# Kernel optimization log

Measured on AMD Instinct MI355X. Metric: run time of the kernel, lower is better.

Reference implementation:

```python
import jax, jax.numpy as jnp
import numpy as np

N_NODES = 100000


def setup_inputs() -> dict:
    key = jax.random.key(0)
    ks = jax.random.split(key, 6)
    x = jax.random.normal(ks[0], (N_NODES, 128), dtype=jnp.float32)
    edge_index = jax.random.randint(ks[1], (2, 1600000), 0, N_NODES, dtype=jnp.int32)
    W_gcn = jax.random.normal(ks[2], (128, 128), dtype=jnp.float32) * 0.05
    b_gcn = jax.random.normal(ks[3], (128,), dtype=jnp.float32) * 0.05
    W_fc = jax.random.normal(ks[4], (64, 128), dtype=jnp.float32) * 0.05
    b_fc = jax.random.normal(ks[5], (64,), dtype=jnp.float32) * 0.05
    return {"x": x, "edge_index": edge_index, "W_gcn": W_gcn, "b_gcn": b_gcn, "W_fc": W_fc, "b_fc": b_fc}


def _gcn_conv(x, edge_index, W, b):
    N = x.shape[0]
    # add self-loops (PyG GCNConv default add_self_loops=True)
    loops = jnp.arange(N, dtype=edge_index.dtype)
    row = jnp.concatenate([edge_index[0], loops])  # source
    col = jnp.concatenate([edge_index[1], loops])  # target (aggregation index)
    # symmetric normalization: deg computed at target with unit edge weights
    deg = jax.ops.segment_sum(jnp.ones_like(col, dtype=x.dtype), col, num_segments=N)
    deg_inv_sqrt = jnp.where(deg > 0, jax.lax.rsqrt(deg), 0.0)
    norm = deg_inv_sqrt[row] * deg_inv_sqrt[col]  # [E+N]
    xw = x @ W  # [N, nhid] - transform before aggregation
    msgs = norm[:, None] * xw[row]  # gather + scale, [E+N, nhid]
    out = jax.ops.segment_sum(msgs, col, num_segments=N)  # scatter-add
    return out + b


def reference(x, edge_index, W_gcn, b_gcn, W_fc, b_fc):
    h = _gcn_conv(x, edge_index, W_gcn, b_gcn)  # [N, nhid]
    return h @ W_fc.T + b_fc  # [N, nclass]
```

## Files before the change

kernel.cpp:

```cpp
#include <hip/hip_runtime.h>
#include <hip/hip_bf16.h>

typedef __hip_bfloat16 bf16;

#define N_NODES 100000
#define N_EDGES 1600000
#define F_IN    128
#define F_OUT   64
#define NBLK    391

#define NB_BKT   196
#define BKT_SH   9
#define BKT_CAP  8960
#define LBIN_CAP 56
#define EPB_A    4096


__device__ __forceinline__ float ldf(const void* p, size_t i, bool isbf) {
    return isbf ? __bfloat162float(((const bf16*)p)[i]) : ((const float*)p)[i];
}
__device__ __forceinline__ void stf(void* p, size_t i, bool isbf, float v) {
    if (isbf) ((bf16*)p)[i] = __float2bfloat16(v);
    else      ((float*)p)[i] = v;
}
__device__ __forceinline__ unsigned short f2bfu(float f) {
    __hip_bfloat16 h = __float2bfloat16(f);
    union { __hip_bfloat16 h; unsigned short u; } c; c.h = h; return c.u;
}
__device__ __forceinline__ float bflo(unsigned int u) { return __uint_as_float(u << 16); }
__device__ __forceinline__ float bfhi(unsigned int u) { return __uint_as_float(u & 0xffff0000u); }

__global__ void k_detect(const unsigned short* __restrict__ w, int* __restrict__ flag) {
    int l = threadIdx.x;
    int good = 0;
#pragma unroll
    for (int q = 0; q < 2; ++q) {
        unsigned short v = w[2 * (l + 64 * q)];
        int e = (v >> 7) & 0xFF;
        if ((e >= 100 && e <= 140) || ((v & 0x7FFF) == 0)) good++;
    }
    unsigned long long m1 = __ballot(good >= 1), m2 = __ballot(good >= 2);
    if (l == 0) *flag = (__popcll(m1) + __popcll(m2) >= 96) ? 1 : 0;
}

__global__ void k_weights(const int* __restrict__ flag,
                          const void* __restrict__ Wg, const void* __restrict__ bg,
                          const void* __restrict__ Wf, const void* __restrict__ bfc,
                          float* __restrict__ M, float* __restrict__ cvec) {
    bool isbf = (*flag != 0);
    int t = blockIdx.x * blockDim.x + threadIdx.x;
    if (t >= F_IN * F_OUT) return;
    int k = t >> 6, c = t & 63;
    float s = 0.f;
    for (int j = 0; j < F_IN; ++j)
        s += ldf(Wg, k * F_IN + j, isbf) * ldf(Wf, c * F_IN + j, isbf);
    M[k * F_OUT + c] = s;
    if (k == 0) {
        float cs = ldf(bfc, c, isbf);
        for (int j = 0; j < F_IN; ++j)
            cs += ldf(bg, j, isbf) * ldf(Wf, c * F_IN + j, isbf);
        cvec[c] = cs;
    }
}


__global__ void k_zero(int* __restrict__ gtail) {
    int i = threadIdx.x;
    if (i < NB_BKT) gtail[i] = 0;
}

__global__ __launch_bounds__(256) void k_binA(const int* __restrict__ ei,
                                              int* __restrict__ gtail,
                                              unsigned* __restrict__ bkt) {
    __shared__ unsigned lbin[NB_BKT * LBIN_CAP];
    __shared__ int lcnt[NB_BKT];
    __shared__ int lbase[NB_BKT];
    int t = threadIdx.x;
    for (int b = t; b < NB_BKT; b += 256) lcnt[b] = 0;
    __syncthreads();
    int e0 = blockIdx.x * EPB_A;
#pragma unroll
    for (int q = 0; q < EPB_A / 256; ++q) {
        int e = e0 + q * 256 + t;
        if (e < N_EDGES) {
            int r = ei[e], c = ei[N_EDGES + e];
            int b = c >> BKT_SH;
            unsigned val = (unsigned)r | ((unsigned)(c & ((1 << BKT_SH) - 1)) << 17);
            int p = atomicAdd(&lcnt[b], 1);
            if (p < LBIN_CAP) {
                lbin[b * LBIN_CAP + p] = val;
            } else {
                int gp = atomicAdd(&gtail[b], 1);
                if (gp < BKT_CAP) bkt[(size_t)b * BKT_CAP + gp] = val;
            }
        }
    }
    __syncthreads();
    for (int b = t; b < NB_BKT; b += 256) {
        int n = min(lcnt[b], LBIN_CAP);
        lbase[b] = atomicAdd(&gtail[b], n);
    }
    __syncthreads();
    int w = t >> 6, l = t & 63;
    for (int b = w; b < NB_BKT; b += 4) {
        int nB = min(lcnt[b], LBIN_CAP);
        int gp0 = lbase[b];
        for (int i = l; i < nB; i += 64) {
            int gp = gp0 + i;
            if (gp < BKT_CAP) bkt[(size_t)b * BKT_CAP + gp] = lbin[b * LBIN_CAP + i];
        }
    }
}

__global__ void k_bktscan(const int* __restrict__ gtail, int* __restrict__ bbase) {
    __shared__ int sm[256];
    int t = threadIdx.x;
    int v = (t < NB_BKT) ? min(gtail[t], BKT_CAP) : 0;
    sm[t] = v; __syncthreads();
    for (int s = 1; s < 256; s <<= 1) {
        int add = (t >= s) ? sm[t - s] : 0;
        __syncthreads();
        sm[t] += add;
        __syncthreads();
    }
    if (t < NB_BKT) bbase[t] = sm[t] - v;
}

__global__ __launch_bounds__(512) void k_build(const unsigned* __restrict__ bkt,
                                               const int* __restrict__ gtail,
                                               const int* __restrict__ bbase,
                                               int* __restrict__ ptr,
                                               int* __restrict__ cnt,
                                               float* __restrict__ dinv,
                                               int* __restrict__ srcs) {
    __shared__ int cntl[512], sm[512], fill[512];
    int b = blockIdx.x, t = threadIdx.x;
    int n = min(gtail[b], BKT_CAP);
    int base = bbase[b];
    cntl[t] = 0;
    __syncthreads();
    for (int i = t; i < n; i += 512)
        atomicAdd(&cntl[bkt[(size_t)b * BKT_CAP + i] >> 17], 1);
    __syncthreads();
    int v = cntl[t];
    sm[t] = v; __syncthreads();
    for (int s = 1; s < 512; s <<= 1) {
        int add = (t >= s) ? sm[t - s] : 0;
        __syncthreads();
        sm[t] += add;
        __syncthreads();
    }
    int excl = sm[t] - v;
    fill[t] = excl;
    int node = (b << BKT_SH) + t;
    if (node < N_NODES) {
        ptr[node]  = base + excl;
        cnt[node]  = v;
        dinv[node] = rsqrtf((float)(v + 1));
    }
    __syncthreads();
    for (int i = t; i < n; i += 512) {
        unsigned e = bkt[(size_t)b * BKT_CAP + i];
        int c = (int)(e >> 17);
        int p = atomicAdd(&fill[c], 1);
        srcs[base + p] = (int)(e & 0x1FFFF);
    }
}

__global__ __launch_bounds__(256) void k_xmz(const int* __restrict__ flag,
                                             const void* __restrict__ x,
                                             const float* __restrict__ M,
                                             const float* __restrict__ dinv,
                                             bf16* __restrict__ y) {
    __shared__ float4 Ms4[F_IN * 16];
    __shared__ float4 xs4[32 * 64];
    int t = threadIdx.x;
    bool isbf = (*flag != 0);
    int r0 = blockIdx.x * 64;

#pragma unroll
    for (int q = 0; q < 8; ++q) {
        int i = q * 256 + t;
        Ms4[i] = ((const float4*)M)[i];
    }
    if (isbf) {
        const unsigned short* xb = (const unsigned short*)x;
#pragma unroll
        for (int q = 0; q < 4; ++q) {
            int idx = q * 256 + t;
            int row = idx >> 4, c8 = idx & 15;
            int rr = min(r0 + row, N_NODES - 1);
            uint4 u = ((const uint4*)(xb + (size_t)rr * F_IN))[c8];
            float4 v0 = make_float4(bflo(u.x), bfhi(u.x), bflo(u.y), bfhi(u.y));
            float4 v1 = make_float4(bflo(u.z), bfhi(u.z), bflo(u.w), bfhi(u.w));
            int k40 = c8 * 2, k41 = c8 * 2 + 1;
            xs4[k40 * 64 + (row ^ (k40 & 7))] = v0;
            xs4[k41 * 64 + (row ^ (k41 & 7))] = v1;
        }
    } else {
        const float* xf = (const float*)x;
#pragma unroll
        for (int q = 0; q < 8; ++q) {
            int idx = q * 256 + t;
            int row = idx >> 5, k4 = idx & 31;
            int rr = min(r0 + row, N_NODES - 1);
            float4 v = ((const float4*)(xf + (size_t)rr * F_IN))[k4];
            xs4[k4 * 64 + (row ^ (k4 & 7))] = v;
        }
    }
    __syncthreads();

    int cg = t & 15;
    int rs = t >> 4;
    float4 a0 = {0,0,0,0}, a1 = {0,0,0,0}, a2 = {0,0,0,0}, a3 = {0,0,0,0};

    for (int k4 = 0; k4 < 32; ++k4) {
        float4 m0 = Ms4[(k4 * 4 + 0) * 16 + cg];
        float4 m1 = Ms4[(k4 * 4 + 1) * 16 + cg];
        float4 m2 = Ms4[(k4 * 4 + 2) * 16 + cg];
        float4 m3 = Ms4[(k4 * 4 + 3) * 16 + cg];
        int sw = k4 & 7;
#pragma unroll
        for (int i = 0; i < 4; ++i) {
            int row = rs * 4 + i;
            float4 xv = xs4[k4 * 64 + (row ^ sw)];
            float4* a = (i == 0) ? &a0 : (i == 1) ? &a1 : (i == 2) ? &a2 : &a3;
            a->x += xv.x * m0.x + xv.y * m1.x + xv.z * m2.x + xv.w * m3.x;
            a->y += xv.x * m0.y + xv.y * m1.y + xv.z * m2.y + xv.w * m3.y;
            a->z += xv.x * m0.z + xv.y * m1.z + xv.z * m2.z + xv.w * m3.z;
            a->w += xv.x * m0.w + xv.y * m1.w + xv.z * m2.w + xv.w * m3.w;
        }
    }

    float4 av[4] = {a0, a1, a2, a3};
#pragma unroll
    for (int i = 0; i < 4; ++i) {
        int row = r0 + rs * 4 + i;
        if (row < N_NODES) {
            float d = dinv[row];
            ushort4 pk;
            pk.x = f2bfu(av[i].x * d); pk.y = f2bfu(av[i].y * d);
            pk.z = f2bfu(av[i].z * d); pk.w = f2bfu(av[i].w * d);
            ((ushort4*)((unsigned short*)y + (size_t)row * F_OUT))[cg] = pk;
        }
    }
}

__global__ __launch_bounds__(256) void k_agg(const int* __restrict__ flag,
                                             const int* __restrict__ ptr,
                                             const int* __restrict__ cnt,
                                             const int* __restrict__ srcs,
                                             const float* __restrict__ dinv,
                                             const bf16* __restrict__ y,
                                             const float* __restrict__ cvec,
                                             void* __restrict__ out) {
    int wid  = (blockIdx.x * 256 + threadIdx.x) >> 6;
    int lane = threadIdx.x & 63;
    int g  = lane >> 3;
    int j8 = lane & 7;
    int node = wid * 8 + g;
    bool alive = node < N_NODES;
    int n = 0, start = 0;
    if (alive) { n = cnt[node]; start = ptr[node]; }
    const uint4* y4 = (const uint4*)y;

    float acc[8];
#pragma unroll
    for (int i = 0; i < 8; ++i) acc[i] = 0.f;

    for (int b = 0; __any(b < n); b += 8) {
        int s = 0;
        int idx = b + j8;
        if (idx < n) s = srcs[start + idx];
#pragma unroll
        for (int k = 0; k < 8; ++k) {
            int su = __shfl(s, (g << 3) | k, 64);
            if (b + k < n) {
                uint4 v = y4[(size_t)su * 8 + j8];
                acc[0] += bflo(v.x); acc[1] += bfhi(v.x);
                acc[2] += bflo(v.y); acc[3] += bfhi(v.y);
                acc[4] += bflo(v.z); acc[5] += bfhi(v.z);
                acc[6] += bflo(v.w); acc[7] += bfhi(v.w);
            }
        }
    }

    if (!alive) return;
    bool isbf = (*flag != 0);
    uint4 sv = y4[(size_t)node * 8 + j8];
    float dn = dinv[node];
    const float4* cv4 = (const float4*)cvec;
    float4 c0 = cv4[j8 * 2], c1 = cv4[j8 * 2 + 1];
    size_t ob = (size_t)node * F_OUT + j8 * 8;
    if (isbf) {
        ushort4 p0, p1;
        p0.x = f2bfu(dn * (acc[0] + bflo(sv.x)) + c0.x);
        p0.y = f2bfu(dn * (acc[1] + bfhi(sv.x)) + c0.y);
        p0.z = f2bfu(dn * (acc[2] + bflo(sv.y)) + c0.z);
        p0.w = f2bfu(dn * (acc[3] + bfhi(sv.y)) + c0.w);
        p1.x = f2bfu(dn * (acc[4] + bflo(sv.z)) + c1.x);
        p1.y = f2bfu(dn * (acc[5] + bfhi(sv.z)) + c1.y);
        p1.z = f2bfu(dn * (acc[6] + bflo(sv.w)) + c1.z);
        p1.w = f2bfu(dn * (acc[7] + bfhi(sv.w)) + c1.w);
        ushort4* ob4 = (ushort4*)((unsigned short*)out + ob);
        ob4[0] = p0; ob4[1] = p1;
    } else {
        float4 q0, q1;
        q0.x = dn * (acc[0] + bflo(sv.x)) + c0.x;
        q0.y = dn * (acc[1] + bfhi(sv.x)) + c0.y;
        q0.z = dn * (acc[2] + bflo(sv.y)) + c0.z;
        q0.w = dn * (acc[3] + bfhi(sv.y)) + c0.w;
        q1.x = dn * (acc[4] + bflo(sv.z)) + c1.x;
        q1.y = dn * (acc[5] + bfhi(sv.z)) + c1.y;
        q1.z = dn * (acc[6] + bflo(sv.w)) + c1.z;
        q1.w = dn * (acc[7] + bfhi(sv.w)) + c1.w;
        float4* of4 = (float4*)((float*)out + ob);
        of4[0] = q0; of4[1] = q1;
    }
}


__global__ void k_init_deg(float* __restrict__ deg) {
    int i = blockIdx.x * blockDim.x + threadIdx.x;
    if (i < N_NODES) deg[i] = 1.0f;
}
__global__ void k_deg(const int* __restrict__ col, float* __restrict__ deg) {
    int e = blockIdx.x * blockDim.x + threadIdx.x;
    if (e < N_EDGES) atomicAdd(&deg[col[e]], 1.0f);
}
__global__ void k_dinv(float* __restrict__ deg) {
    int i = blockIdx.x * blockDim.x + threadIdx.x;
    if (i < N_NODES) deg[i] = rsqrtf(deg[i]);
}
__global__ __launch_bounds__(256) void k_xm(const int* __restrict__ flag,
                                            const void* __restrict__ x,
                                            const float* __restrict__ M,
                                            void* __restrict__ z) {
    __shared__ float Ms[F_IN * F_OUT];
    int t = threadIdx.x;
    for (int i = t; i < F_IN * F_OUT; i += 256) Ms[i] = M[i];
    __syncthreads();
    bool isbf = (*flag != 0);
    int r = blockIdx.x * 4 + (t >> 6);
    int c = t & 63;
    if (r >= N_NODES) return;
    float s = 0.f;
    if (isbf) {
        const bf16* xr = (const bf16*)x + (size_t)r * F_IN;
#pragma unroll
        for (int k = 0; k < F_IN; ++k) s += __bfloat162float(xr[k]) * Ms[k * F_OUT + c];
    } else {
        const float* xr = (const float*)x + (size_t)r * F_IN;
#pragma unroll
        for (int k = 0; k < F_IN; ++k) s += xr[k] * Ms[k * F_OUT + c];
    }
    stf(z, (size_t)r * F_OUT + c, isbf, s);
}
template <int LOGF>
__global__ __launch_bounds__(256) void k_init_acc(const int* __restrict__ flag,
                                                  const float* __restrict__ dinv,
                                                  const void* __restrict__ z,
                                                  float* __restrict__ acc, int base) {
    bool isbf = (*flag != 0);
    int t = blockIdx.x * 256 + threadIdx.x;
    int i = t >> LOGF, f = t & ((1 << LOGF) - 1);
    if (i >= N_NODES) return;
    float d = dinv[i];
    acc[t] = d * d * ldf(z, (size_t)i * F_OUT + base + f, isbf);
}
template <int LOGF>
__global__ __launch_bounds__(256) void k_scatter(const int* __restrict__ flag,
                                                 const int* __restrict__ ei,
                                                 const float* __restrict__ dinv,
                                                 const void* __restrict__ z,
                                                 float* __restrict__ acc, int base) {
    bool isbf = (*flag != 0);
    long long t = (long long)blockIdx.x * 256 + threadIdx.x;
    int e = (int)(t >> LOGF), f = (int)(t & ((1 << LOGF) - 1));
    if (e >= N_EDGES) return;
    int r = ei[e], c = ei[N_EDGES + e];
    float nm = dinv[r] * dinv[c];
    float v  = nm * ldf(z, (size_t)r * F_OUT + base + f, isbf);
    atomicAdd(&acc[((size_t)c << LOGF) + f], v);
}
template <int LOGF>
__global__ __launch_bounds__(256) void k_final(const int* __restrict__ flag,
                                               const float* __restrict__ acc,
                                               const float* __restrict__ cvec,
                                               void* __restrict__ out, int base) {
    bool isbf = (*flag != 0);
    int t = blockIdx.x * 256 + threadIdx.x;
    int i = t >> LOGF, f = t & ((1 << LOGF) - 1);
    if (i >= N_NODES) return;
    stf(out, (size_t)i * F_OUT + base + f, isbf, acc[t] + cvec[base + f]);
}
template <int LOGF>
static void run_passes(const int* flag, const int* ei, const float* dinv,
                       const void* z, float* acc, const float* cvec, void* out,
                       hipStream_t stream) {
    const int fpp = 1 << LOGF;
    const long long tn = (long long)N_NODES * fpp;
    const long long te = (long long)N_EDGES * fpp;
    const int gn = (int)((tn + 255) / 256);
    const int ge = (int)((te + 255) / 256);
    for (int base = 0; base < F_OUT; base += fpp) {
        k_init_acc<LOGF><<<gn, 256, 0, stream>>>(flag, dinv, z, acc, base);
        k_scatter<LOGF><<<ge, 256, 0, stream>>>(flag, ei, dinv, z, acc, base);
        k_final<LOGF><<<gn, 256, 0, stream>>>(flag, acc, cvec, out, base);
    }
}

extern "C" void kernel_launch(void* const* d_in, const int* in_sizes, int n_in,
                              void* d_out, int out_size, void* d_ws, size_t ws_size,
                              hipStream_t stream) {
    const void* x   = d_in[0];
    const int*  ei  = (const int*)d_in[1];
    const void* Wg  = d_in[2];
    const void* bg  = d_in[3];
    const void* Wf  = d_in[4];
    const void* bfc = d_in[5];
    char* ws = (char*)d_ws;

    const size_t CSR_NEED = 20838400;
    if (ws_size >= CSR_NEED) {
        int*      flag  = (int*)(ws + 0);
        float*    dinv  = (float*)(ws + 256);
        float*    M     = (float*)(ws + 400384);
        float*    cvec  = (float*)(ws + 433152);
        int*      cnt   = (int*)(ws + 433664);
        int*      ptr   = (int*)(ws + 833664);
        int*      gtail = (int*)(ws + 1233664);
        int*      bbase = (int*)(ws + 1234560);
        int*      srcs  = (int*)(ws + 1238528);
        bf16*     y     = (bf16*)(ws + 8038400);
        unsigned* bkt   = (unsigned*)(ws + 8038400);

        k_detect<<<1, 64, 0, stream>>>((const unsigned short*)x, flag);
        k_zero<<<1, 256, 0, stream>>>(gtail);
        k_weights<<<(F_IN * F_OUT) / 256, 256, 0, stream>>>(flag, Wg, bg, Wf, bfc, M, cvec);
        k_binA<<<(N_EDGES + EPB_A - 1) / EPB_A, 256, 0, stream>>>(ei, gtail, bkt);
        k_bktscan<<<1, 256, 0, stream>>>(gtail, bbase);
        k_build<<<NB_BKT, 512, 0, stream>>>(bkt, gtail, bbase, ptr, cnt, dinv, srcs);
        k_xmz<<<(N_NODES + 63) / 64, 256, 0, stream>>>(flag, x, M, dinv, y);
        k_agg<<<3125, 256, 0, stream>>>(flag, ptr, cnt, srcs, dinv, y, cvec, d_out);
    } else {
        int*   flag = (int*)(ws + 0);
        float* deg  = (float*)(ws + 256);
        float* M    = (float*)(ws + 400384);
        float* cvec = (float*)(ws + 433152);
        float* acc  = (float*)(ws + 433664);

        k_detect<<<1, 64, 0, stream>>>((const unsigned short*)x, flag);
        k_init_deg<<<NBLK, 256, 0, stream>>>(deg);
        k_deg<<<N_EDGES / 256, 256, 0, stream>>>(ei + N_EDGES, deg);
        k_dinv<<<NBLK, 256, 0, stream>>>(deg);
        k_weights<<<(F_IN * F_OUT) / 256, 256, 0, stream>>>(flag, Wg, bg, Wf, bfc, M, cvec);
        k_xm<<<N_NODES / 4, 256, 0, stream>>>(flag, x, M, d_out);
        const size_t bn = 433664;
        if      (ws_size >= bn + (400000ull << 6)) run_passes<6>(flag, ei, deg, d_out, acc, cvec, d_out, stream);
        else if (ws_size >= bn + (400000ull << 5)) run_passes<5>(flag, ei, deg, d_out, acc, cvec, d_out, stream);
        else if (ws_size >= bn + (400000ull << 4)) run_passes<4>(flag, ei, deg, d_out, acc, cvec, d_out, stream);
        else if (ws_size >= bn + (400000ull << 3)) run_passes<3>(flag, ei, deg, d_out, acc, cvec, d_out, stream);
        else if (ws_size >= bn + (400000ull << 2)) run_passes<2>(flag, ei, deg, d_out, acc, cvec, d_out, stream);
        else if (ws_size >= bn + (400000ull << 1)) run_passes<1>(flag, ei, deg, d_out, acc, cvec, d_out, stream);
        else                                       run_passes<0>(flag, ei, deg, d_out, acc, cvec, d_out, stream);
    }
}
```

Baseline: 234.9 us.

## Use bf16 MFMA with hi/lo split weights for the x@M projection

Adds an MFMA-based projection kernel for bf16 inputs. It multiplies x by the fused weight matrix, storing that matrix as a high and low bf16 pair pre-swizzled into fragment layout so the result keeps near-fp32 accuracy. The goal is to replace the shared-memory FMA path with matrix-core instructions and drop the LDS staging. The old kernel now runs only for fp32 input, and both kernels are launched, so one extra launch of an early-exit kernel is added.

```diff
diff --git a/kernel.cpp b/kernel.cpp
--- a/kernel.cpp
+++ b/kernel.cpp
@@ -16,6 +16,9 @@
 #define EPB_A    4096
 
 
+typedef __attribute__((ext_vector_type(8))) short vbf8;
+typedef __attribute__((ext_vector_type(4))) float vf4;
+
 __device__ __forceinline__ float ldf(const void* p, size_t i, bool isbf) {
     return isbf ? __bfloat162float(((const bf16*)p)[i]) : ((const float*)p)[i];
 }
@@ -46,7 +49,8 @@
 __global__ void k_weights(const int* __restrict__ flag,
                           const void* __restrict__ Wg, const void* __restrict__ bg,
                           const void* __restrict__ Wf, const void* __restrict__ bfc,
-                          float* __restrict__ M, float* __restrict__ cvec) {
+                          float* __restrict__ M, float* __restrict__ cvec,
+                          bf16* __restrict__ Mhi, bf16* __restrict__ Mlo) {
     bool isbf = (*flag != 0);
     int t = blockIdx.x * blockDim.x + threadIdx.x;
     if (t >= F_IN * F_OUT) return;
@@ -55,6 +59,13 @@
     for (int j = 0; j < F_IN; ++j)
         s += ldf(Wg, k * F_IN + j, isbf) * ldf(Wf, c * F_IN + j, isbf);
     M[k * F_OUT + c] = s;
+    if (Mhi) {
+        int l    = (((k >> 3) & 3) << 4) | (c & 15);
+        int fidx = ((((k >> 5) << 2) + (c >> 4)) * 64 + l) * 8 + (k & 7);
+        bf16 h  = __float2bfloat16(s);
+        Mhi[fidx] = h;
+        Mlo[fidx] = __float2bfloat16(s - __bfloat162float(h));
+    }
     if (k == 0) {
         float cs = ldf(bfc, c, isbf);
         for (int j = 0; j < F_IN; ++j)
@@ -167,15 +178,61 @@
     }
 }
 
+__global__ __launch_bounds__(256) void k_xmz_mfma(const int* __restrict__ flag,
+                                                  const void* __restrict__ x,
+                                                  const bf16* __restrict__ Mhi,
+                                                  const bf16* __restrict__ Mlo,
+                                                  const float* __restrict__ dinv,
+                                                  bf16* __restrict__ y) {
+    if (*flag == 0) return;
+    int t = threadIdx.x;
+    int w = t >> 6, lane = t & 63;
+    int g = lane >> 4, cb = lane & 15;
+    int r0 = blockIdx.x * 64 + w * 16;
+    int rr = min(r0 + cb, N_NODES - 1);
+    const vbf8* X8 = (const vbf8*)x;
+    const vbf8* Bh = (const vbf8*)Mhi;
+    const vbf8* Bl = (const vbf8*)Mlo;
+    vf4 acc0 = {0.f,0.f,0.f,0.f}, acc1 = {0.f,0.f,0.f,0.f};
+    vf4 acc2 = {0.f,0.f,0.f,0.f}, acc3 = {0.f,0.f,0.f,0.f};
+#pragma unroll
+    for (int kk = 0; kk < 4; ++kk) {
+        vbf8 a = X8[(size_t)rr * 16 + kk * 4 + g];
+        int bb = kk * 256 + lane;
+        acc0 = __builtin_amdgcn_mfma_f32_16x16x32_bf16(a, Bh[bb      ], acc0, 0, 0, 0);
+        acc0 = __builtin_amdgcn_mfma_f32_16x16x32_bf16(a, Bl[bb      ], acc0, 0, 0, 0);
+        acc1 = __builtin_amdgcn_mfma_f32_16x16x32_bf16(a, Bh[bb +  64], acc1, 0, 0, 0);
+        acc1 = __builtin_amdgcn_mfma_f32_16x16x32_bf16(a, Bl[bb +  64], acc1, 0, 0, 0);
+        acc2 = __builtin_amdgcn_mfma_f32_16x16x32_bf16(a, Bh[bb + 128], acc2, 0, 0, 0);
+        acc2 = __builtin_amdgcn_mfma_f32_16x16x32_bf16(a, Bl[bb + 128], acc2, 0, 0, 0);
+        acc3 = __builtin_amdgcn_mfma_f32_16x16x32_bf16(a, Bh[bb + 192], acc3, 0, 0, 0);
+        acc3 = __builtin_amdgcn_mfma_f32_16x16x32_bf16(a, Bl[bb + 192], acc3, 0, 0, 0);
+    }
+    unsigned short* yb = (unsigned short*)y;
+#pragma unroll
+    for (int i = 0; i < 4; ++i) {
+        int r = r0 + g * 4 + i;
+        if (r < N_NODES) {
+            float d = dinv[r];
+            unsigned short* yr = yb + (size_t)r * F_OUT + cb;
+            yr[0]  = f2bfu(acc0[i] * d);
+            yr[16] = f2bfu(acc1[i] * d);
+            yr[32] = f2bfu(acc2[i] * d);
+            yr[48] = f2bfu(acc3[i] * d);
+        }
+    }
+}
+
 __global__ __launch_bounds__(256) void k_xmz(const int* __restrict__ flag,
                                              const void* __restrict__ x,
                                              const float* __restrict__ M,
                                              const float* __restrict__ dinv,
                                              bf16* __restrict__ y) {
+    if (*flag != 0) return;
     __shared__ float4 Ms4[F_IN * 16];
     __shared__ float4 xs4[32 * 64];
     int t = threadIdx.x;
-    bool isbf = (*flag != 0);
+    bool isbf = false;
     int r0 = blockIdx.x * 64;
 
 #pragma unroll
@@ -421,7 +478,7 @@
     const void* bfc = d_in[5];
     char* ws = (char*)d_ws;
 
-    const size_t CSR_NEED = 20838400;
+    const size_t CSR_NEED = 20871168;
     if (ws_size >= CSR_NEED) {
         int*      flag  = (int*)(ws + 0);
         float*    dinv  = (float*)(ws + 256);
@@ -434,13 +491,16 @@
         int*      srcs  = (int*)(ws + 1238528);
         bf16*     y     = (bf16*)(ws + 8038400);
         unsigned* bkt   = (unsigned*)(ws + 8038400);
+        bf16*     Mhi   = (bf16*)(ws + 20838400);
+        bf16*     Mlo   = (bf16*)(ws + 20854784);
 
         k_detect<<<1, 64, 0, stream>>>((const unsigned short*)x, flag);
         k_zero<<<1, 256, 0, stream>>>(gtail);
-        k_weights<<<(F_IN * F_OUT) / 256, 256, 0, stream>>>(flag, Wg, bg, Wf, bfc, M, cvec);
+        k_weights<<<(F_IN * F_OUT) / 256, 256, 0, stream>>>(flag, Wg, bg, Wf, bfc, M, cvec, Mhi, Mlo);
         k_binA<<<(N_EDGES + EPB_A - 1) / EPB_A, 256, 0, stream>>>(ei, gtail, bkt);
         k_bktscan<<<1, 256, 0, stream>>>(gtail, bbase);
         k_build<<<NB_BKT, 512, 0, stream>>>(bkt, gtail, bbase, ptr, cnt, dinv, srcs);
+        k_xmz_mfma<<<(N_NODES + 63) / 64, 256, 0, stream>>>(flag, x, Mhi, Mlo, dinv, y);
         k_xmz<<<(N_NODES + 63) / 64, 256, 0, stream>>>(flag, x, M, dinv, y);
         k_agg<<<3125, 256, 0, stream>>>(flag, ptr, cnt, srcs, dinv, y, cvec, d_out);
     } else {
@@ -454,7 +514,7 @@
         k_init_deg<<<NBLK, 256, 0, stream>>>(deg);
         k_deg<<<N_EDGES / 256, 256, 0, stream>>>(ei + N_EDGES, deg);
         k_dinv<<<NBLK, 256, 0, stream>>>(deg);
-        k_weights<<<(F_IN * F_OUT) / 256, 256, 0, stream>>>(flag, Wg, bg, Wf, bfc, M, cvec);
+        k_weights<<<(F_IN * F_OUT) / 256, 256, 0, stream>>>(flag, Wg, bg, Wf, bfc, M, cvec, (bf16*)nullptr, (bf16*)nullptr);
         k_xm<<<N_NODES / 4, 256, 0, stream>>>(flag, x, M, d_out);
         const size_t bn = 433664;
         if      (ws_size >= bn + (400000ull << 6)) run_passes<6>(flag, ei, deg, d_out, acc, cvec, d_out, stream);
```

Measured after the change: 239.3 us. No clear change (+1.9%).
